# Performance work log

Measured on AMD Instinct MI355X. Metric: run time of the kernel, lower is better.

Reference implementation:

```python
import jax, jax.numpy as jnp
import numpy as np

EMBED_DIM = 2048
NUM_HEADS = 16
HEAD_DIM = EMBED_DIM // NUM_HEADS
B, S = 1, 2048


def rotate_half(x):
    x1, x2 = jnp.split(x, 2, axis=-1)
    return jnp.concatenate((-x2, x1), axis=-1)


def setup_inputs() -> dict:
    key = jax.random.key(0)
    ks = jax.random.split(key, 8)
    scale = 1.0 / np.sqrt(EMBED_DIM)
    x = jax.random.normal(ks[0], (B, S, EMBED_DIM), dtype=jnp.float32)
    # realistic RoPE tables
    inv_freq = 1.0 / (10000.0 ** (jnp.arange(0, HEAD_DIM, 2, dtype=jnp.float32) / HEAD_DIM))
    t = jnp.arange(S, dtype=jnp.float32)
    freqs = jnp.outer(t, inv_freq)                      # [S, D/2]
    emb = jnp.concatenate((freqs, freqs), axis=-1)      # [S, D]
    rotary_cos = jnp.broadcast_to(jnp.cos(emb)[None], (B, S, HEAD_DIM))
    rotary_sin = jnp.broadcast_to(jnp.sin(emb)[None], (B, S, HEAD_DIM))
    Wq = jax.random.normal(ks[1], (EMBED_DIM, EMBED_DIM), dtype=jnp.float32) * scale
    Wk = jax.random.normal(ks[2], (EMBED_DIM, EMBED_DIM), dtype=jnp.float32) * scale
    Wv = jax.random.normal(ks[3], (EMBED_DIM, EMBED_DIM), dtype=jnp.float32) * scale
    Wo = jax.random.normal(ks[4], (EMBED_DIM, EMBED_DIM), dtype=jnp.float32) * scale
    return {"x": x, "rotary_cos": rotary_cos, "rotary_sin": rotary_sin,
            "Wq": Wq, "Wk": Wk, "Wv": Wv, "Wo": Wo}


def reference(x, rotary_cos, rotary_sin, Wq, Wk, Wv, Wo):
    b, s, e = x.shape
    h, d = NUM_HEADS, HEAD_DIM
    # QKV projections (nn.Linear: x @ W.T), reshape to [B, H, S, D]
    def proj(W):
        return jnp.einsum('bse,fe->bsf', x, W).reshape(b, s, h, d).transpose(0, 2, 1, 3)
    q, k, v = proj(Wq), proj(Wk), proj(Wv)
    # RoPE: cos/sin [B, S, D] -> [B, 1, S, D]
    cos = rotary_cos[:, None, :, :]
    sin = rotary_sin[:, None, :, :]
    q = q * cos + rotate_half(q) * sin
    k = k * cos + rotate_half(k) * sin
    # causal SDPA
    scores = jnp.einsum('bhqd,bhkd->bhqk', q, k) / jnp.sqrt(jnp.float32(d)).astype(x.dtype)
    causal = jnp.tril(jnp.ones((s, s), dtype=bool))
    scores = jnp.where(causal, scores, jnp.finfo(scores.dtype).min)
    attn = jax.nn.softmax(scores, axis=-1)
    out = jnp.einsum('bhqk,bhkd->bhqd', attn, v)
    out = out.transpose(0, 2, 1, 3).reshape(b, s, e)
    return jnp.einsum('bse,fe->bsf', out, Wo)
```

## Files before the change

kernel.cpp:

```cpp
#include <hip/hip_runtime.h>
#include <hip/hip_bf16.h>

#define S_LEN 2048
#define EMB   2048
#define NH    16
#define HD    128

typedef __attribute__((ext_vector_type(8))) __bf16 bf16x8;
typedef __attribute__((ext_vector_type(8))) unsigned short ushort8;
typedef __attribute__((ext_vector_type(4))) unsigned short ushort4v;
typedef __attribute__((ext_vector_type(4))) float  floatx4;

__device__ inline unsigned short f2b(float f) {
    __hip_bfloat16 h = __float2bfloat16(f);
    return *reinterpret_cast<unsigned short*>(&h);
}
__device__ inline float b2f(unsigned short u) {
    union { unsigned int i; float f; } c;
    c.i = ((unsigned int)u) << 16;
    return c.f;
}

__device__ inline ushort8 cvt16_lo(const float4& a, const float4& b) {
    ushort8 r;
    r[0] = f2b(a.x); r[1] = f2b(a.y); r[2] = f2b(a.z); r[3] = f2b(a.w);
    r[4] = f2b(b.x); r[5] = f2b(b.y); r[6] = f2b(b.z); r[7] = f2b(b.w);
    return r;
}

__device__ inline void gll16(const unsigned short* g, unsigned short* l) {
    __builtin_amdgcn_global_load_lds(
        (const __attribute__((address_space(1))) unsigned int*)g,
        (__attribute__((address_space(3))) unsigned int*)l, 16, 0, 0);
}

__global__ __launch_bounds__(256) void cvt_bf16x5(
    const float* __restrict__ s0, const float* __restrict__ s1,
    const float* __restrict__ s2, const float* __restrict__ s3,
    const float* __restrict__ s4,
    unsigned short* __restrict__ d0, unsigned short* __restrict__ d1,
    unsigned short* __restrict__ d2, unsigned short* __restrict__ d3,
    unsigned short* __restrict__ d4)
{
    const int i = blockIdx.x * 256 + threadIdx.x;
    const float* s; unsigned short* d;
    switch (blockIdx.y) {
        case 0: s = s0; d = d0; break;
        case 1: s = s1; d = d1; break;
        case 2: s = s2; d = d2; break;
        case 3: s = s3; d = d3; break;
        default: s = s4; d = d4; break;
    }
    float4 v = ((const float4*)s)[i];
    ushort4v r;
    r[0] = f2b(v.x); r[1] = f2b(v.y); r[2] = f2b(v.z); r[3] = f2b(v.w);
    ((ushort4v*)d)[i] = r;
}


__global__ __launch_bounds__(256) void gemm_qkv_async(
    const unsigned short* __restrict__ Ab,
    const unsigned short* __restrict__ Bq, const unsigned short* __restrict__ Bk,
    const unsigned short* __restrict__ Bv,
    __hip_bfloat16* __restrict__ qbuf, __hip_bfloat16* __restrict__ kbuf,
    __hip_bfloat16* __restrict__ vT,
    const float* __restrict__ rc, const float* __restrict__ rs)
{
    __shared__ __align__(16) union {
        struct { unsigned short A[8192]; unsigned short B[8192]; } s;
        unsigned short CtV[128][136];
        unsigned short CtR[128][137];
    } sm;

    const int m0   = blockIdx.x * 128;
    const int by   = blockIdx.y;
    const int widx = by >> 4;
    const int hh   = by & 15;
    const int n0   = hh * 128;
    const unsigned short* Bb = (widx == 0) ? Bq : (widx == 1) ? Bk : Bv;

    const int t    = threadIdx.x;
    const int lane = t & 63;
    const int w    = t >> 6;
    const int l15  = lane & 15;
    const int g4   = lane >> 4;
    const int mw   = (w >> 1) * 64;
    const int nw   = (w & 1) * 64;

    const int rl = lane >> 3;
    const int cl = ((lane & 7) ^ rl) * 8;

    const floatx4 z = {0.f, 0.f, 0.f, 0.f};
    floatx4 acc[4][4];
    #pragma unroll
    for (int i = 0; i < 4; i++)
        #pragma unroll
        for (int j = 0; j < 4; j++) acc[i][j] = z;

    const int K = EMB;
    for (int k0 = 0; k0 < K; k0 += 64) {
        __syncthreads();
        #pragma unroll
        for (int c = 0; c < 4; c++) {
            const int ck  = w * 4 + c;
            const int row = ck * 8 + rl;
            gll16(Ab + (size_t)(m0 + row) * K + k0 + cl, &sm.s.A[ck * 512]);
            gll16(Bb + (size_t)(n0 + row) * K + k0 + cl, &sm.s.B[ck * 512]);
        }
        __syncthreads();

        #pragma unroll
        for (int s = 0; s < 2; s++) {
            bf16x8 af[4], bg[4];
            #pragma unroll
            for (int i = 0; i < 4; i++)
                af[i] = *(const bf16x8*)&sm.s.A[(mw + i * 16 + l15) * 64
                                                + (((s * 4 + g4) ^ (l15 & 7)) * 8)];
            #pragma unroll
            for (int j = 0; j < 4; j++)
                bg[j] = *(const bf16x8*)&sm.s.B[(nw + j * 16 + l15) * 64
                                                + (((s * 4 + g4) ^ (l15 & 7)) * 8)];
            #pragma unroll
            for (int i = 0; i < 4; i++)
                #pragma unroll
                for (int j = 0; j < 4; j++)
                    acc[i][j] = __builtin_amdgcn_mfma_f32_16x16x32_bf16(af[i], bg[j], acc[i][j], 0, 0, 0);
        }
    }

    if (widx < 2) {
        __syncthreads();
        #pragma unroll
        for (int i = 0; i < 4; i++)
            #pragma unroll
            for (int j = 0; j < 4; j++)
                #pragma unroll
                for (int r = 0; r < 4; r++)
                    sm.CtR[nw + j * 16 + l15][mw + i * 16 + g4 * 4 + r] = f2b(acc[i][j][r]);
        __syncthreads();

        __hip_bfloat16* dst = (widx == 0) ? qbuf : kbuf;
        const int dd  = t & 127;
        const int sl0 = t >> 7;
        #pragma unroll 4
        for (int rep = 0; rep < 64; rep++) {
            const int sl = rep * 2 + sl0;
            const int s  = m0 + sl;
            const float c  = rc[(size_t)s * HD + dd];
            const float sn = rs[(size_t)s * HD + dd];
            const float x0 = b2f(sm.CtR[dd][sl]);
            const float xr = b2f(sm.CtR[dd ^ 64][sl]);
            const float rot = (dd < 64) ? -xr : xr;
            dst[((size_t)hh * S_LEN + s) * HD + dd] = __float2bfloat16(x0 * c + rot * sn);
        }
    } else {
        __syncthreads();
        #pragma unroll
        for (int i = 0; i < 4; i++)
            #pragma unroll
            for (int j = 0; j < 4; j++)
                #pragma unroll
                for (int r = 0; r < 4; r++)
                    sm.CtV[nw + j * 16 + l15][mw + i * 16 + g4 * 4 + r] = f2b(acc[i][j][r]);
        __syncthreads();
        const int dd = t >> 1;
        const int ms = (t & 1) * 64;
        __hip_bfloat16* dstv = vT + ((size_t)hh * HD + dd) * S_LEN + m0 + ms;
        #pragma unroll
        for (int c = 0; c < 8; c++)
            *(ushort8*)(dstv + c * 8) = *(const ushort8*)&sm.CtV[dd][ms + c * 8];
    }
}

__global__ __launch_bounds__(256) void gemm_wo_async(
    const unsigned short* __restrict__ Ab,
    const unsigned short* __restrict__ Bb,
    float* __restrict__ outMN)
{
    __shared__ __align__(16) struct { unsigned short A[8192]; unsigned short B[8192]; } sm;

    const int m0 = blockIdx.x * 128;
    const int n0 = blockIdx.y * 128;
    const int kz = blockIdx.z;

    const int t    = threadIdx.x;
    const int lane = t & 63;
    const int w    = t >> 6;
    const int l15  = lane & 15;
    const int g4   = lane >> 4;
    const int mw   = (w >> 1) * 64;
    const int nw   = (w & 1) * 64;

    const int rl = lane >> 3;
    const int cl = ((lane & 7) ^ rl) * 8;

    const floatx4 z = {0.f, 0.f, 0.f, 0.f};
    floatx4 acc[4][4];
    #pragma unroll
    for (int i = 0; i < 4; i++)
        #pragma unroll
        for (int j = 0; j < 4; j++) acc[i][j] = z;

    const int K = EMB;
    const int kbeg = kz * (K / 2), kend = kbeg + K / 2;
    for (int k0 = kbeg; k0 < kend; k0 += 64) {
        __syncthreads();
        #pragma unroll
        for (int c = 0; c < 4; c++) {
            const int ck  = w * 4 + c;
            const int row = ck * 8 + rl;
            gll16(Ab + (size_t)(m0 + row) * K + k0 + cl, &sm.A[ck * 512]);
            gll16(Bb + (size_t)(n0 + row) * K + k0 + cl, &sm.B[ck * 512]);
        }
        __syncthreads();

        #pragma unroll
        for (int s = 0; s < 2; s++) {
            bf16x8 af[4], bg[4];
            #pragma unroll
            for (int i = 0; i < 4; i++)
                af[i] = *(const bf16x8*)&sm.A[(mw + i * 16 + l15) * 64
                                              + (((s * 4 + g4) ^ (l15 & 7)) * 8)];
            #pragma unroll
            for (int j = 0; j < 4; j++)
                bg[j] = *(const bf16x8*)&sm.B[(nw + j * 16 + l15) * 64
                                              + (((s * 4 + g4) ^ (l15 & 7)) * 8)];
            #pragma unroll
            for (int i = 0; i < 4; i++)
                #pragma unroll
                for (int j = 0; j < 4; j++)
                    acc[i][j] = __builtin_amdgcn_mfma_f32_16x16x32_bf16(af[i], bg[j], acc[i][j], 0, 0, 0);
        }
    }

    #pragma unroll
    for (int i = 0; i < 4; i++)
        #pragma unroll
        for (int j = 0; j < 4; j++)
            #pragma unroll
            for (int r = 0; r < 4; r++) {
                const int row = m0 + mw + i * 16 + g4 * 4 + r;
                const int col = n0 + nw + j * 16 + l15;
                atomicAdd(&outMN[(size_t)row * EMB + col], acc[i][j][r]);
            }
}

__global__ __launch_bounds__(256) void flash_attn_sk(
    const __hip_bfloat16* __restrict__ qb, const __hip_bfloat16* __restrict__ kb,
    const __hip_bfloat16* __restrict__ vT,
    unsigned short* __restrict__ O0, unsigned short* __restrict__ O1,
    float* __restrict__ lp0, float* __restrict__ lp1)
{
    __shared__ __align__(16) unsigned short Ks[64][136];
    __shared__ __align__(16) unsigned short Vs[128][72];
    __shared__ __align__(16) unsigned short Ps[4][16][72];

    const int bx = (gridDim.x - 1) - blockIdx.x;
    const int q0 = bx * 64;
    const int h  = blockIdx.y;
    const int zz = blockIdx.z;
    const int T  = bx + 1;
    const int Th = (T + 1) >> 1;
    const int t0 = (zz == 0) ? 0 : Th;
    const int t1 = (zz == 0) ? Th : T;

    const int t    = threadIdx.x;
    const int lane = t & 63;
    const int w    = t >> 6;
    const size_t hb  = (size_t)h * S_LEN;
    const size_t hbT = (size_t)h * HD;

    const int l15 = lane & 15;
    const int g4  = lane >> 4;
    const int koff = g4 * 8;

    const int kr = t >> 2;
    const int kc = (t & 3) * 32;
    const int vr = t >> 1;
    const int vc = (t & 1) * 32;

    bf16x8 qf[4];
    const __hip_bfloat16* qrow = qb + (hb + q0 + w * 16 + l15) * HD;
    #pragma unroll
    for (int kk = 0; kk < 4; kk++)
        qf[kk] = *(const bf16x8*)(qrow + kk * 32 + koff);

    const floatx4 z = {0.f, 0.f, 0.f, 0.f};
    floatx4 O[8] = {z, z, z, z, z, z, z, z};
    float lpart[4] = {0.f, 0.f, 0.f, 0.f};

    const float scale = 0.08838834764831845f;

    ushort8 krg[4], vrg[4];
    if (t0 < t1) {
        const __hip_bfloat16* kg = kb + (hb + t0 * 64 + kr) * HD + kc;
        const __hip_bfloat16* vg = vT + (hbT + vr) * S_LEN + t0 * 64 + vc;
        #pragma unroll
        for (int c = 0; c < 4; c++) krg[c] = *(const ushort8*)(kg + c * 8);
        #pragma unroll
        for (int c = 0; c < 4; c++) vrg[c] = *(const ushort8*)(vg + c * 8);
    }

    for (int ti = t0; ti < t1; ti++) {
        const int jb0 = ti * 64;
        __syncthreads();
        #pragma unroll
        for (int c = 0; c < 4; c++) *(ushort8*)&Ks[kr][kc + c * 8] = krg[c];
        #pragma unroll
        for (int c = 0; c < 4; c++) *(ushort8*)&Vs[vr][vc + c * 8] = vrg[c];
        __syncthreads();

        if (ti + 1 < t1) {
            const __hip_bfloat16* kg = kb + (hb + jb0 + 64 + kr) * HD + kc;
            const __hip_bfloat16* vg = vT + (hbT + vr) * S_LEN + jb0 + 64 + vc;
            #pragma unroll
            for (int c = 0; c < 4; c++) krg[c] = *(const ushort8*)(kg + c * 8);
            #pragma unroll
            for (int c = 0; c < 4; c++) vrg[c] = *(const ushort8*)(vg + c * 8);
        }

        floatx4 sc[4];
        #pragma unroll
        for (int jb = 0; jb < 4; jb++) {
            floatx4 acc = z;
            #pragma unroll
            for (int kk = 0; kk < 4; kk++) {
                bf16x8 kf = *(const bf16x8*)&Ks[jb * 16 + l15][kk * 32 + koff];
                acc = __builtin_amdgcn_mfma_f32_16x16x32_bf16(qf[kk], kf, acc, 0, 0, 0);
            }
            sc[jb] = acc;
        }

        const bool diag = (jb0 == q0);
        #pragma unroll
        for (int jb = 0; jb < 4; jb++)
            #pragma unroll
            for (int r = 0; r < 4; r++) {
                float s = sc[jb][r] * scale;
                if (diag && (jb * 16 + l15) > (w * 16 + g4 * 4 + r)) s = -1e30f;
                float p = __expf(s - 6.0f);
                sc[jb][r] = p;
                lpart[r] += p;
            }

        #pragma unroll
        for (int jb = 0; jb < 4; jb++)
            #pragma unroll
            for (int r = 0; r < 4; r++)
                Ps[w][g4 * 4 + r][jb * 16 + l15] = f2b(sc[jb][r]);

        #pragma unroll
        for (int half = 0; half < 2; half++) {
            bf16x8 af = *(const bf16x8*)&Ps[w][l15][half * 32 + koff];
            #pragma unroll
            for (int db = 0; db < 8; db++) {
                bf16x8 bf = *(const bf16x8*)&Vs[db * 16 + l15][half * 32 + koff];
                O[db] = __builtin_amdgcn_mfma_f32_16x16x32_bf16(af, bf, O[db], 0, 0, 0);
            }
        }
    }

    unsigned short* Oz = zz ? O1 : O0;
    float*          lz = zz ? lp1 : lp0;
    #pragma unroll
    for (int r = 0; r < 4; r++) {
        float s = lpart[r];
        #pragma unroll
        for (int o = 1; o < 16; o <<= 1) s += __shfl_xor(s, o, 64);
        if (l15 == 0)
            lz[(h << 11) + q0 + w * 16 + g4 * 4 + r] = s;
    }

    #pragma unroll
    for (int db = 0; db < 8; db++)
        #pragma unroll
        for (int r = 0; r < 4; r++) {
            const int row = q0 + w * 16 + g4 * 4 + r;
            const int col = h * HD + db * 16 + l15;
            Oz[(size_t)row * EMB + col] = f2b(O[db][r]);
        }
}

__global__ __launch_bounds__(256) void attn_combine(
    const unsigned short* __restrict__ O0, const unsigned short* __restrict__ O1,
    const float* __restrict__ lp0, const float* __restrict__ lp1,
    __hip_bfloat16* __restrict__ attnb)
{
    const int idx  = blockIdx.x * 256 + threadIdx.x;
    const int base = idx * 8;
    const int s    = base >> 11;
    const int col  = base & 2047;
    const int h    = col >> 7;
    const float l  = lp0[(h << 11) + s] + lp1[(h << 11) + s];
    const float inv = 1.f / l;
    ushort8 a = *(const ushort8*)(O0 + base);
    ushort8 b = *(const ushort8*)(O1 + base);
    ushort8 r;
    #pragma unroll
    for (int e = 0; e < 8; e++)
        r[e] = f2b((b2f(a[e]) + b2f(b[e])) * inv);
    *(ushort8*)((unsigned short*)attnb + base) = r;
}

template <int MODE>
__global__ __launch_bounds__(256) void gemm128f(
    const void* __restrict__ Av,
    const void* __restrict__ B0v, const void* __restrict__ B1v,
    const void* __restrict__ B2v,
    float* __restrict__ outMN,
    __hip_bfloat16* __restrict__ qbuf, __hip_bfloat16* __restrict__ kbuf,
    __hip_bfloat16* __restrict__ vT,
    const float* __restrict__ rc, const float* __restrict__ rs)
{
    __shared__ union {
        struct { unsigned short A[128][40]; unsigned short B[128][40]; } s;
        unsigned short CtV[128][136];
        unsigned short CtR[128][137];
    } sm;

    const int m0 = blockIdx.x * 128;
    const int by = blockIdx.y;

    int widx = 0, hh = 0, n0 = 0;
    const void* Bv;
    if (MODE == 1) {
        widx = by >> 4; hh = by & 15; n0 = hh * 128;
        Bv = (widx == 0) ? B0v : (widx == 1) ? B1v : B2v;
    } else { n0 = by * 128; Bv = B0v; }

    const int t = threadIdx.x, lane = t & 63, w = t >> 6;
    const int l15 = lane & 15, g4 = lane >> 4, koff = g4 * 8;
    const int mw = (w >> 1) * 64, nw = (w & 1) * 64;
    const int srow = t >> 1, scol = (t & 1) * 16;

    const floatx4 z = {0.f, 0.f, 0.f, 0.f};
    floatx4 acc[4][4];
    #pragma unroll
    for (int i = 0; i < 4; i++)
        #pragma unroll
        for (int j = 0; j < 4; j++) acc[i][j] = z;

    const int K = EMB;
    for (int k0 = 0; k0 < K; k0 += 32) {
        ushort8 a0, a1, b0, b1;
        if (MODE == 0) {
            const unsigned short* Ab = (const unsigned short*)Av;
            a0 = *(const ushort8*)(Ab + (size_t)(m0 + srow) * K + k0 + scol);
            a1 = *(const ushort8*)(Ab + (size_t)(m0 + srow) * K + k0 + scol + 8);
        } else {
            const float* Af = (const float*)Av;
            const float* ap = Af + (size_t)(m0 + srow) * K + k0 + scol;
            a0 = cvt16_lo(*(const float4*)(ap),     *(const float4*)(ap + 4));
            a1 = cvt16_lo(*(const float4*)(ap + 8), *(const float4*)(ap + 12));
        }
        {
            const float* Bf = (const float*)Bv;
            const float* bp = Bf + (size_t)(n0 + srow) * K + k0 + scol;
            b0 = cvt16_lo(*(const float4*)(bp),     *(const float4*)(bp + 4));
            b1 = cvt16_lo(*(const float4*)(bp + 8), *(const float4*)(bp + 12));
        }
        __syncthreads();
        *(ushort8*)&sm.s.A[srow][scol]     = a0;
        *(ushort8*)&sm.s.A[srow][scol + 8] = a1;
        *(ushort8*)&sm.s.B[srow][scol]     = b0;
        *(ushort8*)&sm.s.B[srow][scol + 8] = b1;
        __syncthreads();

        bf16x8 af[4], bg[4];
        #pragma unroll
        for (int i = 0; i < 4; i++)
            af[i] = *(const bf16x8*)&sm.s.A[mw + i * 16 + l15][koff];
        #pragma unroll
        for (int j = 0; j < 4; j++)
            bg[j] = *(const bf16x8*)&sm.s.B[nw + j * 16 + l15][koff];
        #pragma unroll
        for (int i = 0; i < 4; i++)
            #pragma unroll
            for (int j = 0; j < 4; j++)
                acc[i][j] = __builtin_amdgcn_mfma_f32_16x16x32_bf16(af[i], bg[j], acc[i][j], 0, 0, 0);
    }

    if (MODE == 0) {
        #pragma unroll
        for (int i = 0; i < 4; i++)
            #pragma unroll
            for (int j = 0; j < 4; j++)
                #pragma unroll
                for (int r = 0; r < 4; r++) {
                    int row = m0 + mw + i * 16 + g4 * 4 + r;
                    int col = n0 + nw + j * 16 + l15;
                    outMN[(size_t)row * EMB + col] = acc[i][j][r];
                }
    } else if (widx < 2) {
        __syncthreads();
        #pragma unroll
        for (int i = 0; i < 4; i++)
            #pragma unroll
            for (int j = 0; j < 4; j++)
                #pragma unroll
                for (int r = 0; r < 4; r++)
                    sm.CtR[nw + j * 16 + l15][mw + i * 16 + g4 * 4 + r] = f2b(acc[i][j][r]);
        __syncthreads();
        __hip_bfloat16* dst = (widx == 0) ? qbuf : kbuf;
        const int dd = t & 127, sl0 = t >> 7;
        #pragma unroll 4
        for (int rep = 0; rep < 64; rep++) {
            const int sl = rep * 2 + sl0;
            const int s  = m0 + sl;
            const float c  = rc[(size_t)s * HD + dd];
            const float sn = rs[(size_t)s * HD + dd];
            const float x0 = b2f(sm.CtR[dd][sl]);
            const float xr = b2f(sm.CtR[dd ^ 64][sl]);
            const float rot = (dd < 64) ? -xr : xr;
            dst[((size_t)hh * S_LEN + s) * HD + dd] = __float2bfloat16(x0 * c + rot * sn);
        }
    } else {
        __syncthreads();
        #pragma unroll
        for (int i = 0; i < 4; i++)
            #pragma unroll
            for (int j = 0; j < 4; j++)
                #pragma unroll
                for (int r = 0; r < 4; r++)
                    sm.CtV[nw + j * 16 + l15][mw + i * 16 + g4 * 4 + r] = f2b(acc[i][j][r]);
        __syncthreads();
        const int dd = t >> 1, ms = (t & 1) * 64;
        __hip_bfloat16* dstv = vT + ((size_t)hh * HD + dd) * S_LEN + m0 + ms;
        #pragma unroll
        for (int c = 0; c < 8; c++)
            *(ushort8*)(dstv + c * 8) = *(const ushort8*)&sm.CtV[dd][ms + c * 8];
    }
}

__global__ __launch_bounds__(256) void flash_attn(
    const __hip_bfloat16* __restrict__ qb, const __hip_bfloat16* __restrict__ kb,
    const __hip_bfloat16* __restrict__ vT, __hip_bfloat16* __restrict__ attnb)
{
    __shared__ __align__(16) unsigned short Ks[64][136];
    __shared__ __align__(16) unsigned short Vs[128][72];
    __shared__ __align__(16) unsigned short Ps[4][16][72];

    const int bx = (gridDim.x - 1) - blockIdx.x;
    const int q0 = bx * 64;
    const int h  = blockIdx.y;
    const int t    = threadIdx.x;
    const int lane = t & 63;
    const int w    = t >> 6;
    const size_t hb  = (size_t)h * S_LEN;
    const size_t hbT = (size_t)h * HD;

    const int l15 = lane & 15;
    const int g4  = lane >> 4;
    const int koff = g4 * 8;

    const int kr = t >> 2;
    const int kc = (t & 3) * 32;
    const int vr = t >> 1;
    const int vc = (t & 1) * 32;

    bf16x8 qf[4];
    const __hip_bfloat16* qrow = qb + (hb + q0 + w * 16 + l15) * HD;
    #pragma unroll
    for (int kk = 0; kk < 4; kk++)
        qf[kk] = *(const bf16x8*)(qrow + kk * 32 + koff);

    const floatx4 z = {0.f, 0.f, 0.f, 0.f};
    floatx4 O[8] = {z, z, z, z, z, z, z, z};
    float lpart[4] = {0.f, 0.f, 0.f, 0.f};

    const float scale = 0.08838834764831845f;

    ushort8 krg[4], vrg[4];
    {
        const __hip_bfloat16* kg = kb + (hb + kr) * HD + kc;
        const __hip_bfloat16* vg = vT + (hbT + vr) * S_LEN + vc;
        #pragma unroll
        for (int c = 0; c < 4; c++) krg[c] = *(const ushort8*)(kg + c * 8);
        #pragma unroll
        for (int c = 0; c < 4; c++) vrg[c] = *(const ushort8*)(vg + c * 8);
    }

    for (int jb0 = 0; jb0 <= q0; jb0 += 64) {
        __syncthreads();
        #pragma unroll
        for (int c = 0; c < 4; c++) *(ushort8*)&Ks[kr][kc + c * 8] = krg[c];
        #pragma unroll
        for (int c = 0; c < 4; c++) *(ushort8*)&Vs[vr][vc + c * 8] = vrg[c];
        __syncthreads();

        if (jb0 + 64 <= q0) {
            const __hip_bfloat16* kg = kb + (hb + jb0 + 64 + kr) * HD + kc;
            const __hip_bfloat16* vg = vT + (hbT + vr) * S_LEN + jb0 + 64 + vc;
            #pragma unroll
            for (int c = 0; c < 4; c++) krg[c] = *(const ushort8*)(kg + c * 8);
            #pragma unroll
            for (int c = 0; c < 4; c++) vrg[c] = *(const ushort8*)(vg + c * 8);
        }

        floatx4 sc[4];
        #pragma unroll
        for (int jb = 0; jb < 4; jb++) {
            floatx4 acc = z;
            #pragma unroll
            for (int kk = 0; kk < 4; kk++) {
                bf16x8 kf = *(const bf16x8*)&Ks[jb * 16 + l15][kk * 32 + koff];
                acc = __builtin_amdgcn_mfma_f32_16x16x32_bf16(qf[kk], kf, acc, 0, 0, 0);
            }
            sc[jb] = acc;
        }

        const bool diag = (jb0 == q0);
        #pragma unroll
        for (int jb = 0; jb < 4; jb++)
            #pragma unroll
            for (int r = 0; r < 4; r++) {
                float s = sc[jb][r] * scale;
                if (diag && (jb * 16 + l15) > (w * 16 + g4 * 4 + r)) s = -1e30f;
                float p = __expf(s - 6.0f);
                sc[jb][r] = p;
                lpart[r] += p;
            }

        #pragma unroll
        for (int jb = 0; jb < 4; jb++)
            #pragma unroll
            for (int r = 0; r < 4; r++)
                Ps[w][g4 * 4 + r][jb * 16 + l15] = f2b(sc[jb][r]);

        #pragma unroll
        for (int half = 0; half < 2; half++) {
            bf16x8 af = *(const bf16x8*)&Ps[w][l15][half * 32 + koff];
            #pragma unroll
            for (int db = 0; db < 8; db++) {
                bf16x8 bf = *(const bf16x8*)&Vs[db * 16 + l15][half * 32 + koff];
                O[db] = __builtin_amdgcn_mfma_f32_16x16x32_bf16(af, bf, O[db], 0, 0, 0);
            }
        }
    }

    float inv[4];
    #pragma unroll
    for (int r = 0; r < 4; r++) {
        float s = lpart[r];
        #pragma unroll
        for (int o = 1; o < 16; o <<= 1) s += __shfl_xor(s, o, 64);
        inv[r] = 1.f / s;
    }

    #pragma unroll
    for (int db = 0; db < 8; db++)
        #pragma unroll
        for (int r = 0; r < 4; r++) {
            const int row = q0 + w * 16 + g4 * 4 + r;
            const int col = h * HD + db * 16 + l15;
            attnb[(size_t)row * EMB + col] = __float2bfloat16(O[db][r] * inv[r]);
        }
}

extern "C" void kernel_launch(void* const* d_in, const int* in_sizes, int n_in,
                              void* d_out, int out_size, void* d_ws, size_t ws_size,
                              hipStream_t stream) {
    const float* x  = (const float*)d_in[0];
    const float* rc = (const float*)d_in[1];
    const float* rs = (const float*)d_in[2];
    const float* Wq = (const float*)d_in[3];
    const float* Wk = (const float*)d_in[4];
    const float* Wv = (const float*)d_in[5];
    const float* Wo = (const float*)d_in[6];
    float* out = (float*)d_out;

    const size_t MB = 1u << 20;
    char* ws = (char*)d_ws;
    __hip_bfloat16* qbuf  = (__hip_bfloat16*)(ws);
    __hip_bfloat16* kbuf  = (__hip_bfloat16*)(ws +  8 * MB);
    __hip_bfloat16* vTbuf = (__hip_bfloat16*)(ws + 16 * MB);
    __hip_bfloat16* attnb = (__hip_bfloat16*)(ws + 24 * MB);

    const bool pre = (ws_size >= 72 * MB);

    if (pre) {
        unsigned short* xb  = (unsigned short*)(ws + 32 * MB);
        unsigned short* wqb = (unsigned short*)(ws + 40 * MB);
        unsigned short* wkb = (unsigned short*)(ws + 48 * MB);
        unsigned short* wvb = (unsigned short*)(ws + 56 * MB);
        unsigned short* wob = (unsigned short*)(ws + 64 * MB);
        unsigned short* Op0 = xb;
        unsigned short* Op1 = wqb;
        float*          lp0 = (float*)wkb;
        float*          lp1 = (float*)(ws + 48 * MB + 256 * 1024);

        hipMemsetAsync(out, 0, (size_t)S_LEN * EMB * sizeof(float), stream);

        hipLaunchKernelGGL(cvt_bf16x5, dim3(4096, 5), dim3(256), 0, stream,
                           x, Wq, Wk, Wv, Wo, xb, wqb, wkb, wvb, wob);

        hipLaunchKernelGGL(gemm_qkv_async, dim3(16, 48), dim3(256), 0, stream,
                           xb, wqb, wkb, wvb, qbuf, kbuf, vTbuf, rc, rs);

        hipLaunchKernelGGL(flash_attn_sk, dim3(S_LEN / 64, NH, 2), dim3(256), 0, stream,
                           qbuf, kbuf, vTbuf, Op0, Op1, lp0, lp1);

        hipLaunchKernelGGL(attn_combine, dim3(2048), dim3(256), 0, stream,
                           Op0, Op1, lp0, lp1, attnb);

        hipLaunchKernelGGL(gemm_wo_async, dim3(16, 16, 2), dim3(256), 0, stream,
                           (const unsigned short*)attnb, wob, out);
    } else {
        hipLaunchKernelGGL((gemm128f<1>), dim3(16, 48), dim3(256), 0, stream,
                           (const void*)x, (const void*)Wq, (const void*)Wk,
                           (const void*)Wv, (float*)nullptr,
                           qbuf, kbuf, vTbuf, rc, rs);

        hipLaunchKernelGGL(flash_attn, dim3(S_LEN / 64, NH), dim3(256), 0, stream,
                           qbuf, kbuf, vTbuf, attnb);

        hipLaunchKernelGGL((gemm128f<0>), dim3(16, 16), dim3(256), 0, stream,
                           (const void*)attnb, (const void*)Wo, (const void*)nullptr,
                           (const void*)nullptr, out,
                           (__hip_bfloat16*)nullptr, (__hip_bfloat16*)nullptr,
                           (__hip_bfloat16*)nullptr, rc, rs);
    }
}
```

Before: 328.6 us.

## Shrink GEMM K-tile to 32 and replace split-K atomics in Wo GEMM

Both the QKV and output-projection GEMMs now stage 32-wide K slices instead of 64-wide, with a new 4-chunk XOR swizzle, which halves shared memory per block and may allow more resident blocks. The Wo GEMM drops split-K with atomicAdd and the memset of the output. It instead uses 128x64 tiles over the full K range and writes results directly. The cost is twice as many barrier-separated loop iterations with fewer MFMAs between syncs, and smaller output tiles that reload more of the A operand.

```diff
diff --git a/kernel.cpp b/kernel.cpp
--- a/kernel.cpp
+++ b/kernel.cpp
@@ -67,7 +67,7 @@
     const float* __restrict__ rc, const float* __restrict__ rs)
 {
     __shared__ __align__(16) union {
-        struct { unsigned short A[8192]; unsigned short B[8192]; } s;
+        struct { unsigned short A[4096]; unsigned short B[4096]; } s;
         unsigned short CtV[128][136];
         unsigned short CtR[128][137];
     } sm;
@@ -87,8 +87,9 @@
     const int mw   = (w >> 1) * 64;
     const int nw   = (w & 1) * 64;
 
-    const int rl = lane >> 3;
-    const int cl = ((lane & 7) ^ rl) * 8;
+    const int crow = lane >> 2;
+    const int clog = (lane & 3) ^ ((crow >> 1) & 3);
+    const int pc   = g4 ^ ((l15 >> 1) & 3);
 
     const floatx4 z = {0.f, 0.f, 0.f, 0.f};
     floatx4 acc[4][4];
@@ -98,34 +99,30 @@
         for (int j = 0; j < 4; j++) acc[i][j] = z;
 
     const int K = EMB;
-    for (int k0 = 0; k0 < K; k0 += 64) {
-        __syncthreads();
-        #pragma unroll
-        for (int c = 0; c < 4; c++) {
-            const int ck  = w * 4 + c;
-            const int row = ck * 8 + rl;
-            gll16(Ab + (size_t)(m0 + row) * K + k0 + cl, &sm.s.A[ck * 512]);
-            gll16(Bb + (size_t)(n0 + row) * K + k0 + cl, &sm.s.B[ck * 512]);
-        }
-        __syncthreads();
-
-        #pragma unroll
-        for (int s = 0; s < 2; s++) {
-            bf16x8 af[4], bg[4];
-            #pragma unroll
-            for (int i = 0; i < 4; i++)
-                af[i] = *(const bf16x8*)&sm.s.A[(mw + i * 16 + l15) * 64
-                                                + (((s * 4 + g4) ^ (l15 & 7)) * 8)];
+    for (int k0 = 0; k0 < K; k0 += 32) {
+        __syncthreads();
+        #pragma unroll
+        for (int c = 0; c < 2; c++) {
+            const int ck  = w * 2 + c;
+            const int row = ck * 16 + crow;
+            gll16(Ab + (size_t)(m0 + row) * K + k0 + clog * 8, &sm.s.A[ck * 512]);
+            gll16(Bb + (size_t)(n0 + row) * K + k0 + clog * 8, &sm.s.B[ck * 512]);
+        }
+        __syncthreads();
+
+        bf16x8 af[4], bg[4];
+        #pragma unroll
+        for (int i = 0; i < 4; i++)
+            af[i] = *(const bf16x8*)&sm.s.A[(mw + i * 16 + l15) * 32 + pc * 8];
+        #pragma unroll
+        for (int j = 0; j < 4; j++)
+            bg[j] = *(const bf16x8*)&sm.s.B[(nw + j * 16 + l15) * 32 + pc * 8];
+
+        #pragma unroll
+        for (int i = 0; i < 4; i++)
             #pragma unroll
             for (int j = 0; j < 4; j++)
-                bg[j] = *(const bf16x8*)&sm.s.B[(nw + j * 16 + l15) * 64
-                                                + (((s * 4 + g4) ^ (l15 & 7)) * 8)];
-            #pragma unroll
-            for (int i = 0; i < 4; i++)
-                #pragma unroll
-                for (int j = 0; j < 4; j++)
-                    acc[i][j] = __builtin_amdgcn_mfma_f32_16x16x32_bf16(af[i], bg[j], acc[i][j], 0, 0, 0);
-        }
+                acc[i][j] = __builtin_amdgcn_mfma_f32_16x16x32_bf16(af[i], bg[j], acc[i][j], 0, 0, 0);
     }
 
     if (widx < 2) {
@@ -177,11 +174,10 @@
     const unsigned short* __restrict__ Bb,
     float* __restrict__ outMN)
 {
-    __shared__ __align__(16) struct { unsigned short A[8192]; unsigned short B[8192]; } sm;
+    __shared__ __align__(16) struct { unsigned short A[4096]; unsigned short B[2048]; } sm;
 
     const int m0 = blockIdx.x * 128;
-    const int n0 = blockIdx.y * 128;
-    const int kz = blockIdx.z;
+    const int n0 = blockIdx.y * 64;
 
     const int t    = threadIdx.x;
     const int lane = t & 63;
@@ -189,59 +185,58 @@
     const int l15  = lane & 15;
     const int g4   = lane >> 4;
     const int mw   = (w >> 1) * 64;
-    const int nw   = (w & 1) * 64;
-
-    const int rl = lane >> 3;
-    const int cl = ((lane & 7) ^ rl) * 8;
+    const int nw   = (w & 1) * 32;
+
+    const int crow = lane >> 2;
+    const int clog = (lane & 3) ^ ((crow >> 1) & 3);
+    const int pc   = g4 ^ ((l15 >> 1) & 3);
 
     const floatx4 z = {0.f, 0.f, 0.f, 0.f};
-    floatx4 acc[4][4];
+    floatx4 acc[4][2];
     #pragma unroll
     for (int i = 0; i < 4; i++)
         #pragma unroll
-        for (int j = 0; j < 4; j++) acc[i][j] = z;
+        for (int j = 0; j < 2; j++) acc[i][j] = z;
 
     const int K = EMB;
-    const int kbeg = kz * (K / 2), kend = kbeg + K / 2;
-    for (int k0 = kbeg; k0 < kend; k0 += 64) {
-        __syncthreads();
-        #pragma unroll
-        for (int c = 0; c < 4; c++) {
-            const int ck  = w * 4 + c;
-            const int row = ck * 8 + rl;
-            gll16(Ab + (size_t)(m0 + row) * K + k0 + cl, &sm.A[ck * 512]);
-            gll16(Bb + (size_t)(n0 + row) * K + k0 + cl, &sm.B[ck * 512]);
-        }
-        __syncthreads();
-
-        #pragma unroll
-        for (int s = 0; s < 2; s++) {
-            bf16x8 af[4], bg[4];
-            #pragma unroll
-            for (int i = 0; i < 4; i++)
-                af[i] = *(const bf16x8*)&sm.A[(mw + i * 16 + l15) * 64
-                                              + (((s * 4 + g4) ^ (l15 & 7)) * 8)];
-            #pragma unroll
-            for (int j = 0; j < 4; j++)
-                bg[j] = *(const bf16x8*)&sm.B[(nw + j * 16 + l15) * 64
-                                              + (((s * 4 + g4) ^ (l15 & 7)) * 8)];
-            #pragma unroll
-            for (int i = 0; i < 4; i++)
-                #pragma unroll
-                for (int j = 0; j < 4; j++)
-                    acc[i][j] = __builtin_amdgcn_mfma_f32_16x16x32_bf16(af[i], bg[j], acc[i][j], 0, 0, 0);
-        }
+    for (int k0 = 0; k0 < K; k0 += 32) {
+        __syncthreads();
+        #pragma unroll
+        for (int c = 0; c < 2; c++) {
+            const int ck  = w * 2 + c;
+            const int row = ck * 16 + crow;
+            gll16(Ab + (size_t)(m0 + row) * K + k0 + clog * 8, &sm.A[ck * 512]);
+        }
+        {
+            const int row = w * 16 + crow;
+            gll16(Bb + (size_t)(n0 + row) * K + k0 + clog * 8, &sm.B[w * 512]);
+        }
+        __syncthreads();
+
+        bf16x8 af[4], bg[2];
+        #pragma unroll
+        for (int i = 0; i < 4; i++)
+            af[i] = *(const bf16x8*)&sm.A[(mw + i * 16 + l15) * 32 + pc * 8];
+        #pragma unroll
+        for (int j = 0; j < 2; j++)
+            bg[j] = *(const bf16x8*)&sm.B[(nw + j * 16 + l15) * 32 + pc * 8];
+
+        #pragma unroll
+        for (int i = 0; i < 4; i++)
+            #pragma unroll
+            for (int j = 0; j < 2; j++)
+                acc[i][j] = __builtin_amdgcn_mfma_f32_16x16x32_bf16(af[i], bg[j], acc[i][j], 0, 0, 0);
     }
 
     #pragma unroll
     for (int i = 0; i < 4; i++)
         #pragma unroll
-        for (int j = 0; j < 4; j++)
+        for (int j = 0; j < 2; j++)
             #pragma unroll
             for (int r = 0; r < 4; r++) {
                 const int row = m0 + mw + i * 16 + g4 * 4 + r;
                 const int col = n0 + nw + j * 16 + l15;
-                atomicAdd(&outMN[(size_t)row * EMB + col], acc[i][j][r]);
+                outMN[(size_t)row * EMB + col] = acc[i][j][r];
             }
 }
 
@@ -689,8 +684,6 @@
         float*          lp0 = (float*)wkb;
         float*          lp1 = (float*)(ws + 48 * MB + 256 * 1024);
 
-        hipMemsetAsync(out, 0, (size_t)S_LEN * EMB * sizeof(float), stream);
-
         hipLaunchKernelGGL(cvt_bf16x5, dim3(4096, 5), dim3(256), 0, stream,
                            x, Wq, Wk, Wv, Wo, xb, wqb, wkb, wvb, wob);
 
@@ -703,7 +696,7 @@
         hipLaunchKernelGGL(attn_combine, dim3(2048), dim3(256), 0, stream,
                            Op0, Op1, lp0, lp1, attnb);
 
-        hipLaunchKernelGGL(gemm_wo_async, dim3(16, 16, 2), dim3(256), 0, stream,
+        hipLaunchKernelGGL(gemm_wo_async, dim3(16, 32), dim3(256), 0, stream,
                            (const unsigned short*)attnb, wob, out);
     } else {
         hipLaunchKernelGGL((gemm128f<1>), dim3(16, 48), dim3(256), 0, stream,
```

After: 293.8 us. 10.6% less time.
